# Kernel optimization log

Hardware: AMD Instinct MI355X
Metric: run time of the kernel (lower is better)

Reference implementation:

```python
import jax, jax.numpy as jnp
import numpy as np

N_NODES, N_EDGES, NUM_GRAPHS = 50000, 800000, 64
F_DIM, H_DIM, N_LAYERS, N_CLASSES = 64, 64, 3, 16
EPS = 1e-5  # StdAggregation epsilon (PyG)


def setup_inputs() -> dict:
    key = jax.random.key(0)
    ks = jax.random.split(key, 12)
    s = 0.05
    x = jax.random.normal(ks[0], (N_NODES, F_DIM), jnp.float32)
    edge_index = jax.random.randint(ks[1], (2, N_EDGES), 0, N_NODES, dtype=jnp.int32)
    batch = jnp.sort(jax.random.randint(ks[2], (N_NODES,), 0, NUM_GRAPHS, dtype=jnp.int32))
    # per-layer PNAConv params (towers=1): pre Linear(2F->F), post Linear(13F->H), lin Linear(H->H)
    pre_w = jax.random.normal(ks[3], (N_LAYERS, F_DIM, 2 * F_DIM), jnp.float32) * s
    pre_b = jnp.zeros((N_LAYERS, F_DIM), jnp.float32)
    post_w = jax.random.normal(ks[4], (N_LAYERS, H_DIM, 13 * F_DIM), jnp.float32) * s
    post_b = jnp.zeros((N_LAYERS, H_DIM), jnp.float32)
    lin_w = jax.random.normal(ks[5], (N_LAYERS, H_DIM, H_DIM), jnp.float32) * s
    lin_b = jnp.zeros((N_LAYERS, H_DIM), jnp.float32)
    mlp_w1 = jax.random.normal(ks[6], (H_DIM, H_DIM), jnp.float32) * s
    mlp_b1 = jnp.zeros((H_DIM,), jnp.float32)
    mlp_w2 = jax.random.normal(ks[7], (N_CLASSES, H_DIM), jnp.float32) * s
    mlp_b2 = jnp.zeros((N_CLASSES,), jnp.float32)
    return dict(x=x, edge_index=edge_index, batch=batch,
                pre_w=pre_w, pre_b=pre_b, post_w=post_w, post_b=post_b,
                lin_w=lin_w, lin_b=lin_b, mlp_w1=mlp_w1, mlp_b1=mlp_b1,
                mlp_w2=mlp_w2, mlp_b2=mlp_b2)


def pna_forward(x, src, dst, pre_w, pre_b, post_w, post_b, lin_w, lin_b,
                mlp_w1, mlp_b1, mlp_w2, mlp_b2, batch):
    N = x.shape[0]
    deg_raw = jax.ops.segment_sum(jnp.ones_like(src, jnp.float32), dst, N)  # in-degree [N]
    deg = jnp.maximum(deg_raw, 1.0)[:, None]
    # avg log degree (PNA avg_deg['log'] from the degree histogram of this graph)
    avg_log = jnp.mean(jnp.log(deg_raw + 1.0))
    log_deg = jnp.log(deg + 1.0)
    amp = log_deg / avg_log          # amplification scaler [N,1]
    att = avg_log / log_deg          # attenuation scaler [N,1]
    has_in = (deg_raw > 0)[:, None]

    for l in range(pre_w.shape[0]):
        h = jnp.concatenate([x[dst], x[src]], axis=-1)        # [E, 2F] (x_i, x_j)
        m = h @ pre_w[l].T + pre_b[l]                          # pre_nn message [E, F]
        s1 = jax.ops.segment_sum(m, dst, N)
        s2 = jax.ops.segment_sum(m * m, dst, N)
        mean = s1 / deg
        std = jnp.sqrt(jax.nn.relu(s2 / deg - mean * mean) + EPS)
        mn = jnp.where(has_in, jax.ops.segment_min(m, dst, N), 0.0)
        mx = jnp.where(has_in, jax.ops.segment_max(m, dst, N), 0.0)
        aggr = jnp.concatenate([mean, mn, mx, std], axis=-1)   # [N, 4F]
        out = jnp.concatenate([x, aggr, aggr * amp, aggr * att], axis=-1)  # [N, 13F]
        out = out @ post_w[l].T + post_b[l]                    # post_nn [N, H]
        x = jax.nn.relu(out @ lin_w[l].T + lin_b[l])           # conv.lin + outer ReLU

    # global mean pool over graphs
    counts = jnp.maximum(
        jax.ops.segment_sum(jnp.ones((N,), x.dtype), batch, NUM_GRAPHS), 1.0)
    g = jax.ops.segment_sum(x, batch, NUM_GRAPHS) / counts[:, None]  # [G, H]
    g = jax.nn.relu(g @ mlp_w1.T + mlp_b1)
    return g @ mlp_w2.T + mlp_b2                               # [G, C]


def reference(x, edge_index, batch, pre_w, pre_b, post_w, post_b,
              lin_w, lin_b, mlp_w1, mlp_b1, mlp_w2, mlp_b2):
    src, dst = edge_index[0], edge_index[1]
    return pna_forward(x, src, dst, pre_w, pre_b, post_w, post_b,
                       lin_w, lin_b, mlp_w1, mlp_b1, mlp_w2, mlp_b2, batch)
```

## Files before the change

kernel.cpp:

```cpp
#include <hip/hip_runtime.h>
#include <math.h>

#define N_NODES   50000
#define N_EDGES   800000
#define NUM_GRAPHS 64
#define FDIM      64
#define HDIM      64
#define NLAYERS   3
#define NCLASSES  16
#define EPS       1e-5f

#define SCAN_CHUNK 1024
#define NCHUNKS ((N_NODES + SCAN_CHUNK - 1) / SCAN_CHUNK)

typedef unsigned short u16;
typedef unsigned int   u32;
typedef __attribute__((ext_vector_type(8))) short short8;
typedef __attribute__((ext_vector_type(4))) float floatx4;

#define WKS_LAYER 159744
#define PRES_LAYER 24576

__device__ inline void split1(float f, u16& h, u16& m, u16& l) {
    u32 b  = __float_as_uint(f);
    u32 hb = b & 0xFFFF0000u;
    float r = f - __uint_as_float(hb);
    u32 mb = __float_as_uint(r) & 0xFFFF0000u;
    float r2 = r - __uint_as_float(mb);
    u32 lb = __float_as_uint(r2) & 0xFFFF0000u;
    h = (u16)(hb >> 16); m = (u16)(mb >> 16); l = (u16)(lb >> 16);
}

__device__ inline void gl_lds16(const void* g, void* l) {
    __builtin_amdgcn_global_load_lds(
        (const __attribute__((address_space(1))) u32*)g,
        (__attribute__((address_space(3))) u32*)l, 16, 0, 0);
}

__global__ __launch_bounds__(256) void k_comb(const float* __restrict__ post_w,
                                              const float* __restrict__ lin_w,
                                              const float* __restrict__ pre_w,
                                              const float* __restrict__ post_b,
                                              const float* __restrict__ lin_b,
                                              u16* __restrict__ WkS,
                                              u16* __restrict__ PreS,
                                              float* __restrict__ bcv,
                                              int* __restrict__ cnt,
                                              float* __restrict__ logsum) {
    int b = blockIdx.x, t = threadIdx.x;
    int zi = b * 256 + t;
    if (zi < N_NODES) cnt[zi] = 0;
    if (zi == 0) *logsum = 0.f;

    if (b < 624) {
        int c  = t & 63;
        int kl = t >> 6;
        int l  = b / 208;
        int o  = (b % 208) * 4 + kl;
        const float* lw = lin_w + (size_t)l * 4096 + c * 64;
        const float* pw = post_w + (size_t)l * 53248 + o;
        float acc = 0.f;
        #pragma unroll 8
        for (int j = 0; j < 64; ++j)
            acc += lw[j] * pw[(size_t)j * 832];
        u16 h, m, lo;
        split1(acc, h, m, lo);

        int kn;
        if (o < 64) kn = o;
        else {
            int s  = (o - 64) >> 8;
            int mm = (o - 64) & 255;
            int j  = mm >> 5, r = mm & 31;
            kn = 64 + j * 96 + s * 32 + r;
        }
        int ch  = kn >> 5;
        int kin = kn & 31;
        int n16 = c & 15, nt = c >> 4;
        int swk = (((kin >> 3) + (n16 >> 1)) & 3) * 8 + (kin & 7);
        size_t base = (size_t)l * WKS_LAYER + (size_t)ch * 6144
                    + nt * 512 + n16 * 32 + swk;
        WkS[base]        = h;
        WkS[base + 2048] = m;
        WkS[base + 4096] = lo;
    } else if (b == 624) {
        if (t < 192) {
            int l = t >> 6, c = t & 63;
            float acc = lin_b[l * 64 + c];
            for (int j = 0; j < 64; ++j)
                acc += lin_w[(size_t)l * 4096 + c * 64 + j] * post_b[l * 64 + j];
            bcv[l * 64 + c] = acc;
        }
    } else {
        int i = (b - 625) * 256 + t;
        int l = i >> 13;
        int rem = i & 8191;
        int c128 = rem >> 6;
        int k = rem & 63;
        float v;
        if (c128 < 64) v = pre_w[(size_t)l * 8192 + c128 * 128 + k];
        else           v = pre_w[(size_t)l * 8192 + (c128 - 64) * 128 + 64 + k];
        u16 h, m, lo;
        split1(v, h, m, lo);
        int ch = k >> 5, kin = k & 31;
        int nt = c128 >> 4, n16 = c128 & 15;
        int swk = (((kin >> 3) + (n16 >> 1)) & 3) * 8 + (kin & 7);
        size_t base = (size_t)l * PRES_LAYER + (size_t)ch * 12288
                    + nt * 512 + n16 * 32 + swk;
        PreS[base]        = h;
        PreS[base + 4096] = m;
        PreS[base + 8192] = lo;
    }
}

__global__ void k_count(const int* __restrict__ dst, int* __restrict__ cnt,
                        int* __restrict__ rank) {
    int e = blockIdx.x * 256 + threadIdx.x;
    if (e < N_EDGES) rank[e] = atomicAdd(&cnt[dst[e]], 1);
}

__global__ void k_chunk_sums(const int* __restrict__ cnt, int* __restrict__ bsum,
                             float* __restrict__ logsum) {
    __shared__ int   ired[256];
    __shared__ float lred[256];
    int b = blockIdx.x, t = threadIdx.x;
    int base = b * SCAN_CHUNK;
    int s = 0; float ls = 0.f;
    for (int i = t; i < SCAN_CHUNK; i += 256) {
        int idx = base + i;
        if (idx < N_NODES) {
            int v = cnt[idx];
            s += v;
            ls += logf((float)v + 1.0f);
        }
    }
    ired[t] = s; lred[t] = ls;
    __syncthreads();
    for (int off = 128; off > 0; off >>= 1) {
        if (t < off) { ired[t] += ired[t + off]; lred[t] += lred[t + off]; }
        __syncthreads();
    }
    if (t == 0) { bsum[b] = ired[0]; atomicAdd(logsum, lred[0]); }
}

__global__ void k_scan_top(const int* __restrict__ bsum, int* __restrict__ boff,
                           int* __restrict__ row_start) {
    if (threadIdx.x == 0) {
        int acc = 0;
        for (int i = 0; i < NCHUNKS; ++i) { boff[i] = acc; acc += bsum[i]; }
        row_start[N_NODES] = acc;
    }
}

__global__ void k_scan_chunks(const int* __restrict__ cnt, const int* __restrict__ boff,
                              int* __restrict__ row_start) {
    __shared__ int tsum[256];
    int b = blockIdx.x, t = threadIdx.x;
    int base = b * SCAN_CHUNK + t * 4;
    int v[4]; int s = 0;
    #pragma unroll
    for (int i = 0; i < 4; ++i) {
        int idx = base + i;
        v[i] = (idx < N_NODES) ? cnt[idx] : 0;
        s += v[i];
    }
    tsum[t] = s;
    __syncthreads();
    for (int off = 1; off < 256; off <<= 1) {
        int val = (t >= off) ? tsum[t - off] : 0;
        __syncthreads();
        tsum[t] += val;
        __syncthreads();
    }
    int excl = boff[b] + tsum[t] - s;
    #pragma unroll
    for (int i = 0; i < 4; ++i) {
        int idx = base + i;
        if (idx < N_NODES) row_start[idx] = excl;
        excl += v[i];
    }
}

__global__ void k_scatter(const int* __restrict__ src, const int* __restrict__ dst,
                          const int* __restrict__ rank,
                          const int* __restrict__ row_start,
                          int* __restrict__ csr_src) {
    int e = blockIdx.x * 256 + threadIdx.x;
    if (e < N_EDGES) {
        int d = dst[e];
        csr_src[row_start[d] + rank[e]] = src[e];
    }
}

__global__ void k_scal(const int* __restrict__ cnt, const float* __restrict__ logsum,
                       float* __restrict__ inv_deg, float* __restrict__ ampv,
                       float* __restrict__ attv, float* __restrict__ g_sum,
                       int* __restrict__ g_cnt) {
    int n = blockIdx.x * 256 + threadIdx.x;
    if (blockIdx.x == 0) {
        for (int i = threadIdx.x; i < 4096; i += 256) g_sum[i] = 0.f;
        if (threadIdx.x < 64) g_cnt[threadIdx.x] = 0;
    }
    if (n < N_NODES) {
        float avg = logsum[0] / (float)N_NODES;
        float degf = fmaxf((float)cnt[n], 1.0f);
        inv_deg[n] = 1.0f / degf;
        float ld = logf(degf + 1.0f);
        ampv[n] = ld / avg;
        attv[n] = avg / ld;
    }
}

__global__ __launch_bounds__(256, 4) void k_pre(const float* __restrict__ x,
                                                const u16* __restrict__ PreS,
                                                const float* __restrict__ pre_b,
                                                float* __restrict__ p,
                                                float* __restrict__ q) {
    __shared__ u16 ldsB[2 * 12288];
    int t = threadIdx.x;
    int w = t >> 6;
    int lane = t & 63;
    int m = lane & 15;
    int qh = lane >> 4;
    int rowBase = blockIdx.x * 64;

    int myrow = rowBase + 16 * w + m;
    bool vr = myrow < N_NODES;
    int crow = vr ? myrow : 0;
    const float* xrow = x + (size_t)crow * 64;

    int bo = m * 32 + ((qh + (m >> 1)) & 3) * 8;

    #pragma unroll
    for (int ch = 0; ch < 2; ++ch) {
        const char* g = (const char*)PreS + (size_t)ch * 24576 + w * 6144 + lane * 16;
        char* l = (char*)ldsB + ch * 24576 + w * 6144;
        #pragma unroll
        for (int i = 0; i < 6; ++i)
            gl_lds16(g + i * 1024, l + i * 1024);
    }
    float fa[2][8];
    #pragma unroll
    for (int ch = 0; ch < 2; ++ch) {
        const float* sp = xrow + ch * 32 + qh * 8;
        float4 u0 = *(const float4*)sp;
        float4 u1 = *(const float4*)(sp + 4);
        fa[ch][0] = vr ? u0.x : 0.f; fa[ch][1] = vr ? u0.y : 0.f;
        fa[ch][2] = vr ? u0.z : 0.f; fa[ch][3] = vr ? u0.w : 0.f;
        fa[ch][4] = vr ? u1.x : 0.f; fa[ch][5] = vr ? u1.y : 0.f;
        fa[ch][6] = vr ? u1.z : 0.f; fa[ch][7] = vr ? u1.w : 0.f;
    }
    asm volatile("s_waitcnt vmcnt(0)" ::: "memory");
    __syncthreads();

    floatx4 acc[8] = {};
    #pragma unroll
    for (int ch = 0; ch < 2; ++ch) {
        union { u32 u[4]; short8 s8; } AH, AM, AL;
        #pragma unroll
        for (int i = 0; i < 4; ++i) {
            float f0 = fa[ch][2 * i], f1 = fa[ch][2 * i + 1];
            u32 b0 = __float_as_uint(f0), b1 = __float_as_uint(f1);
            u32 h0 = b0 & 0xFFFF0000u,  h1 = b1 & 0xFFFF0000u;
            float r0 = f0 - __uint_as_float(h0);
            float r1 = f1 - __uint_as_float(h1);
            u32 m0 = __float_as_uint(r0) & 0xFFFF0000u;
            u32 m1 = __float_as_uint(r1) & 0xFFFF0000u;
            float s0 = r0 - __uint_as_float(m0);
            float s1 = r1 - __uint_as_float(m1);
            u32 l0 = __float_as_uint(s0) & 0xFFFF0000u;
            u32 l1 = __float_as_uint(s1) & 0xFFFF0000u;
            AH.u[i] = (h0 >> 16) | h1;
            AM.u[i] = (m0 >> 16) | m1;
            AL.u[i] = (l0 >> 16) | l1;
        }
        const u16* Bb = ldsB + ch * 12288;
        #pragma unroll
        for (int nt = 0; nt < 8; ++nt) {
            short8 bH = *(const short8*)(Bb + nt * 512 + bo);
            short8 bM = *(const short8*)(Bb + 4096 + nt * 512 + bo);
            short8 bL = *(const short8*)(Bb + 8192 + nt * 512 + bo);
            acc[nt] = __builtin_amdgcn_mfma_f32_16x16x32_bf16(AH.s8, bH, acc[nt], 0, 0, 0);
            acc[nt] = __builtin_amdgcn_mfma_f32_16x16x32_bf16(AH.s8, bM, acc[nt], 0, 0, 0);
            acc[nt] = __builtin_amdgcn_mfma_f32_16x16x32_bf16(AM.s8, bH, acc[nt], 0, 0, 0);
            acc[nt] = __builtin_amdgcn_mfma_f32_16x16x32_bf16(AH.s8, bL, acc[nt], 0, 0, 0);
            acc[nt] = __builtin_amdgcn_mfma_f32_16x16x32_bf16(AM.s8, bM, acc[nt], 0, 0, 0);
            acc[nt] = __builtin_amdgcn_mfma_f32_16x16x32_bf16(AL.s8, bH, acc[nt], 0, 0, 0);
        }
    }

    int col = m;
    #pragma unroll
    for (int nt = 0; nt < 8; ++nt) {
        int cbase = (nt & 3) * 16 + col;
        float bias = (nt < 4) ? pre_b[cbase] : 0.f;
        float* outp = (nt < 4) ? p : q;
        #pragma unroll
        for (int reg = 0; reg < 4; ++reg) {
            int grow = rowBase + 16 * w + qh * 4 + reg;
            if (grow < N_NODES)
                outp[(size_t)grow * 64 + cbase] = acc[nt][reg] + bias;
        }
    }
}

__global__ __launch_bounds__(256) void k_aggr(const float* __restrict__ p,
                                              const float* __restrict__ q,
                                              const int* __restrict__ row_start,
                                              const int* __restrict__ csr_src,
                                              const float* __restrict__ inv_deg,
                                              float* __restrict__ aggr) {
    int wid  = (blockIdx.x * 256 + threadIdx.x) >> 6;
    int lane = threadIdx.x & 63;
    if (wid >= N_NODES) return;
    int n = wid;
    int beg = row_start[n], end = row_start[n + 1];
    float sum = 0.f, sq = 0.f;
    float mn = INFINITY, mx = -INFINITY;
    int e = beg;
    for (; e + 7 < end; e += 8) {
        float qv[8];
        #pragma unroll
        for (int u = 0; u < 8; ++u) {
            int s = csr_src[e + u];
            qv[u] = q[(size_t)s * 64 + lane];
        }
        #pragma unroll
        for (int u = 0; u < 8; ++u) {
            float m = qv[u];
            sum += m; sq += m * m;
            mn = fminf(mn, m); mx = fmaxf(mx, m);
        }
    }
    for (; e + 3 < end; e += 4) {
        float qv[4];
        #pragma unroll
        for (int u = 0; u < 4; ++u) {
            int s = csr_src[e + u];
            qv[u] = q[(size_t)s * 64 + lane];
        }
        #pragma unroll
        for (int u = 0; u < 4; ++u) {
            float m = qv[u];
            sum += m; sq += m * m;
            mn = fminf(mn, m); mx = fmaxf(mx, m);
        }
    }
    for (; e < end; ++e) {
        int s = csr_src[e];
        float m = q[(size_t)s * 64 + lane];
        sum += m; sq += m * m;
        mn = fminf(mn, m); mx = fmaxf(mx, m);
    }
    float* a = aggr + (size_t)n * 256;
    if (end <= beg) {
        a[lane]       = 0.f;
        a[64 + lane]  = 0.f;
        a[128 + lane] = 0.f;
        a[192 + lane] = sqrtf(EPS);
    } else {
        float pv = p[n * 64 + lane];
        float id = inv_deg[n];
        float meanq = sum * id;
        float var = fmaxf(sq * id - meanq * meanq, 0.f);
        a[lane]       = pv + meanq;
        a[64 + lane]  = pv + mn;
        a[128 + lane] = pv + mx;
        a[192 + lane] = sqrtf(var + EPS);
    }
}

__global__ __launch_bounds__(256, 4) void k_post(const float* __restrict__ x,
                                                 const float* __restrict__ aggr,
                                                 const float* __restrict__ ampv,
                                                 const float* __restrict__ attv,
                                                 const u16* __restrict__ WkS,
                                                 const float* __restrict__ bc,
                                                 float* __restrict__ xout) {
    __shared__ u16 ldsB[3 * 6144];
    int t = threadIdx.x;
    int w = t >> 6;
    int lane = t & 63;
    int m = lane & 15;
    int qh = lane >> 4;
    int rowBase = blockIdx.x * 64;

    int myrow = rowBase + 16 * w + m;
    bool vr = myrow < N_NODES;
    int crow = vr ? myrow : 0;
    float ampR = vr ? ampv[crow] : 0.f;
    float attR = vr ? attv[crow] : 0.f;
    const float* xrow = x + (size_t)crow * 64;
    const float* arow = aggr + (size_t)crow * 256;

    int bo = m * 32 + ((qh + (m >> 1)) & 3) * 8;

    floatx4 acc[4] = {};
    float fc[8], fn[8];

    auto aptr = [&](int ch) -> const float* {
        if (ch <= 0) return xrow;
        if (ch == 1) return xrow + 32;
        int j = (ch - 2) / 3;
        if (j > 7) j = 7;
        return arow + j * 32;
    };
    auto loadRaw = [&](const float* sp, float* f) {
        float4 u0 = *(const float4*)(sp + qh * 8);
        float4 u1 = *(const float4*)(sp + qh * 8 + 4);
        f[0] = vr ? u0.x : 0.f; f[1] = vr ? u0.y : 0.f;
        f[2] = vr ? u0.z : 0.f; f[3] = vr ? u0.w : 0.f;
        f[4] = vr ? u1.x : 0.f; f[5] = vr ? u1.y : 0.f;
        f[6] = vr ? u1.z : 0.f; f[7] = vr ? u1.w : 0.f;
    };
    auto stageIssue = [&](int ch, int buf) {
        const char* g = (const char*)WkS + (size_t)ch * 12288 + w * 3072 + lane * 16;
        char* l = (char*)ldsB + buf * 12288 + w * 3072;
        #pragma unroll
        for (int i = 0; i < 3; ++i)
            gl_lds16(g + i * 1024, l + i * 1024);
    };

    loadRaw(aptr(0), fc);
    stageIssue(0, 0);
    stageIssue(1, 1);
    asm volatile("s_waitcnt vmcnt(3)" ::: "memory");
    asm volatile("s_barrier" ::: "memory");

    for (int ch = 0; ch < 26; ++ch) {
        loadRaw(aptr(ch + 1), fn);
        int ch2 = (ch + 2 < 26) ? ch + 2 : ch + 2 - 26;
        stageIssue(ch2, (ch + 2) % 3);

        float sc = 1.f;
        if (ch >= 2) {
            int s = (ch - 2) % 3;
            sc = (s == 0) ? 1.f : ((s == 1) ? ampR : attR);
        }

        union { u32 u[4]; short8 s8; } AH, AM, AL;
        #pragma unroll
        for (int i = 0; i < 4; ++i) {
            float f0 = fc[2 * i] * sc, f1 = fc[2 * i + 1] * sc;
            u32 b0 = __float_as_uint(f0), b1 = __float_as_uint(f1);
            u32 h0 = b0 & 0xFFFF0000u,  h1 = b1 & 0xFFFF0000u;
            float r0 = f0 - __uint_as_float(h0);
            float r1 = f1 - __uint_as_float(h1);
            u32 m0 = __float_as_uint(r0) & 0xFFFF0000u;
            u32 m1 = __float_as_uint(r1) & 0xFFFF0000u;
            float s0 = r0 - __uint_as_float(m0);
            float s1 = r1 - __uint_as_float(m1);
            u32 l0 = __float_as_uint(s0) & 0xFFFF0000u;
            u32 l1 = __float_as_uint(s1) & 0xFFFF0000u;
            AH.u[i] = (h0 >> 16) | h1;
            AM.u[i] = (m0 >> 16) | m1;
            AL.u[i] = (l0 >> 16) | l1;
        }

        const u16* Bb = ldsB + (ch % 3) * 6144;
        #pragma unroll
        for (int nt = 0; nt < 4; ++nt) {
            short8 bH = *(const short8*)(Bb + nt * 512 + bo);
            short8 bM = *(const short8*)(Bb + 2048 + nt * 512 + bo);
            short8 bL = *(const short8*)(Bb + 4096 + nt * 512 + bo);
            acc[nt] = __builtin_amdgcn_mfma_f32_16x16x32_bf16(AH.s8, bH, acc[nt], 0, 0, 0);
            acc[nt] = __builtin_amdgcn_mfma_f32_16x16x32_bf16(AH.s8, bM, acc[nt], 0, 0, 0);
            acc[nt] = __builtin_amdgcn_mfma_f32_16x16x32_bf16(AM.s8, bH, acc[nt], 0, 0, 0);
            acc[nt] = __builtin_amdgcn_mfma_f32_16x16x32_bf16(AH.s8, bL, acc[nt], 0, 0, 0);
            acc[nt] = __builtin_amdgcn_mfma_f32_16x16x32_bf16(AM.s8, bM, acc[nt], 0, 0, 0);
            acc[nt] = __builtin_amdgcn_mfma_f32_16x16x32_bf16(AL.s8, bH, acc[nt], 0, 0, 0);
        }

        asm volatile("s_waitcnt vmcnt(5)" ::: "memory");
        asm volatile("s_barrier" ::: "memory");

        #pragma unroll
        for (int i = 0; i < 8; ++i) fc[i] = fn[i];
    }

    int col = lane & 15;
    #pragma unroll
    for (int nt = 0; nt < 4; ++nt) {
        float bias = bc[nt * 16 + col];
        #pragma unroll
        for (int reg = 0; reg < 4; ++reg) {
            int grow = rowBase + 16 * w + qh * 4 + reg;
            if (grow < N_NODES) {
                xout[(size_t)grow * 64 + nt * 16 + col] =
                    fmaxf(acc[nt][reg] + bias, 0.f);
            }
        }
    }
}

__global__ __launch_bounds__(256) void k_pool(const float* __restrict__ x,
                                              const int* __restrict__ batch,
                                              float* __restrict__ g_sum,
                                              int* __restrict__ g_cnt) {
    int lane = threadIdx.x & 63;
    int wave = blockIdx.x * 4 + (threadIdx.x >> 6);
    const int NPW = 16;
    int beg = wave * NPW;
    if (beg >= N_NODES) return;
    int end = min(beg + NPW, N_NODES);
    float acc = 0.f;
    int cur = batch[beg];
    int c = 0;
    for (int n = beg; n < end; ++n) {
        int b = batch[n];
        if (b != cur) {
            atomicAdd(&g_sum[cur * 64 + lane], acc);
            if (lane == 0) atomicAdd(&g_cnt[cur], c);
            acc = 0.f; c = 0; cur = b;
        }
        acc += x[n * 64 + lane];
        ++c;
    }
    atomicAdd(&g_sum[cur * 64 + lane], acc);
    if (lane == 0) atomicAdd(&g_cnt[cur], c);
}

__global__ __launch_bounds__(256) void k_mlp(const float* __restrict__ g_sum,
                                             const int* __restrict__ g_cnt,
                                             const float* __restrict__ w1,
                                             const float* __restrict__ b1,
                                             const float* __restrict__ w2,
                                             const float* __restrict__ b2,
                                             float* __restrict__ out) {
    __shared__ float g[64][64];
    __shared__ float h[64][64];
    __shared__ float wT[64][65];
    int t = threadIdx.x;
    for (int idx = t; idx < 4096; idx += 256) {
        int gi = idx >> 6, c = idx & 63;
        float cntf = fmaxf((float)g_cnt[gi], 1.f);
        g[gi][c] = g_sum[idx] / cntf;
    }
    for (int idx = t; idx < 4096; idx += 256) {
        int c = idx >> 6, k = idx & 63;
        wT[k][c] = w1[c * 64 + k];
    }
    __syncthreads();
    for (int idx = t; idx < 4096; idx += 256) {
        int gi = idx >> 6, c = idx & 63;
        float acc = b1[c];
        for (int k = 0; k < 64; ++k) acc += g[gi][k] * wT[k][c];
        h[gi][c] = fmaxf(acc, 0.f);
    }
    __syncthreads();
    for (int idx = t; idx < 64 * NCLASSES; idx += 256) {
        int gi = idx >> 4, c = idx & 15;
        float acc = b2[c];
        for (int k = 0; k < 64; ++k) acc += h[gi][k] * w2[c * 64 + k];
        out[gi * NCLASSES + c] = acc;
    }
}

extern "C" void kernel_launch(void* const* d_in, const int* in_sizes, int n_in,
                              void* d_out, int out_size, void* d_ws, size_t ws_size,
                              hipStream_t stream) {
    const float* x      = (const float*)d_in[0];
    const int*   ei     = (const int*)d_in[1];
    const int*   batch  = (const int*)d_in[2];
    const float* pre_w  = (const float*)d_in[3];
    const float* pre_b  = (const float*)d_in[4];
    const float* post_w = (const float*)d_in[5];
    const float* post_b = (const float*)d_in[6];
    const float* lin_w  = (const float*)d_in[7];
    const float* lin_b  = (const float*)d_in[8];
    const float* mlp_w1 = (const float*)d_in[9];
    const float* mlp_b1 = (const float*)d_in[10];
    const float* mlp_w2 = (const float*)d_in[11];
    const float* mlp_b2 = (const float*)d_in[12];

    const int* src = ei;
    const int* dst = ei + N_EDGES;

    char* base = (char*)d_ws;
    size_t off = 0;
    auto alloc = [&](size_t bytes) -> void* {
        void* ptr = base + off;
        off += (bytes + 255) & ~(size_t)255;
        return ptr;
    };
    int*   cnt       = (int*)alloc(N_NODES * 4);
    int*   row_start = (int*)alloc((N_NODES + 1) * 4);
    int*   rank      = (int*)alloc(N_EDGES * 4);
    int*   csr_src   = (int*)alloc(N_EDGES * 4);
    int*   bsum      = (int*)alloc(64 * 4);
    int*   boff      = (int*)alloc(64 * 4);
    float* logsum    = (float*)alloc(16);
    float* inv_deg   = (float*)alloc(N_NODES * 4);
    float* ampv      = (float*)alloc(N_NODES * 4);
    float* attv      = (float*)alloc(N_NODES * 4);
    float* p         = (float*)alloc((size_t)N_NODES * 64 * 4);
    float* q         = (float*)alloc((size_t)N_NODES * 64 * 4);
    float* aggr      = (float*)alloc((size_t)N_NODES * 256 * 4);
    float* xb0       = (float*)alloc((size_t)N_NODES * 64 * 4);
    float* xb1       = (float*)alloc((size_t)N_NODES * 64 * 4);
    float* g_sum     = (float*)alloc(64 * 64 * 4);
    int*   g_cnt     = (int*)alloc(64 * 4);
    u16*   WkS       = (u16*)alloc((size_t)3 * WKS_LAYER * 2);
    u16*   PreS      = (u16*)alloc((size_t)3 * PRES_LAYER * 2);
    float* bcv       = (float*)alloc(3 * 64 * 4);

    k_comb<<<721, 256, 0, stream>>>(post_w, lin_w, pre_w, post_b, lin_b,
                                    WkS, PreS, bcv, cnt, logsum);

    k_count<<<(N_EDGES + 255) / 256, 256, 0, stream>>>(dst, cnt, rank);
    k_chunk_sums<<<NCHUNKS, 256, 0, stream>>>(cnt, bsum, logsum);
    k_scan_top<<<1, 64, 0, stream>>>(bsum, boff, row_start);
    k_scan_chunks<<<NCHUNKS, 256, 0, stream>>>(cnt, boff, row_start);
    k_scatter<<<(N_EDGES + 255) / 256, 256, 0, stream>>>(src, dst, rank,
                                                         row_start, csr_src);
    k_scal<<<(N_NODES + 255) / 256, 256, 0, stream>>>(cnt, logsum, inv_deg,
                                                      ampv, attv, g_sum, g_cnt);

    const int GEMM_BLOCKS = (N_NODES + 63) / 64;
    const float* xin = x;
    float* bufs[3] = {xb0, xb1, xb0};
    for (int l = 0; l < NLAYERS; ++l) {
        k_pre<<<GEMM_BLOCKS, 256, 0, stream>>>(xin, PreS + (size_t)l * PRES_LAYER,
                                               pre_b + l * 64, p, q);
        k_aggr<<<(N_NODES + 3) / 4, 256, 0, stream>>>(p, q, row_start, csr_src,
                                                      inv_deg, aggr);
        float* xo = bufs[l];
        k_post<<<GEMM_BLOCKS, 256, 0, stream>>>(xin, aggr, ampv, attv,
                                                WkS + (size_t)l * WKS_LAYER,
                                                bcv + l * 64, xo);
        xin = xo;
    }

    int pool_waves = (N_NODES + 15) / 16;
    k_pool<<<(pool_waves + 3) / 4, 256, 0, stream>>>(xin, batch, g_sum, g_cnt);
    k_mlp<<<1, 256, 0, stream>>>(g_sum, g_cnt, mlp_w1, mlp_b1, mlp_w2, mlp_b2,
                                 (float*)d_out);
}
```

Before: 477.8 us.

## Process two row fragments per wave in post GEMM and defer scaler multiply

The post-aggregation GEMM kernel now handles 128 rows per block, two 16-row fragments per wave, so each staged weight tile in LDS is reused for twice as many rows. The amp/att scaling is no longer applied to the A operand before the bf16 split. Instead three separate accumulators (plain, amp, att) are kept and combined with the per-row scalers in the epilogue, so each aggregate chunk is loaded and split once rather than three times. This raises register pressure (six accumulator arrays), so launch bounds drop to 2 blocks per CU, which may reduce occupancy and latency hiding.

New measurement: 482.3 us. No clear change (+0.9%).

```diff
diff --git a/kernel.cpp b/kernel.cpp
--- a/kernel.cpp
+++ b/kernel.cpp
@@ -370,7 +370,29 @@
     }
 }
 
-__global__ __launch_bounds__(256, 4) void k_post(const float* __restrict__ x,
+#define DOMFMA(ACC0, ACC1)                                                     \
+    {                                                                          \
+        _Pragma("unroll")                                                      \
+        for (int nt = 0; nt < 4; ++nt) {                                       \
+            short8 bH = *(const short8*)(Bb + nt * 512 + bo);                  \
+            short8 bM = *(const short8*)(Bb + 2048 + nt * 512 + bo);           \
+            short8 bL = *(const short8*)(Bb + 4096 + nt * 512 + bo);           \
+            ACC0[nt] = __builtin_amdgcn_mfma_f32_16x16x32_bf16(AH0.s8, bH, ACC0[nt], 0, 0, 0); \
+            ACC0[nt] = __builtin_amdgcn_mfma_f32_16x16x32_bf16(AH0.s8, bM, ACC0[nt], 0, 0, 0); \
+            ACC0[nt] = __builtin_amdgcn_mfma_f32_16x16x32_bf16(AM0.s8, bH, ACC0[nt], 0, 0, 0); \
+            ACC0[nt] = __builtin_amdgcn_mfma_f32_16x16x32_bf16(AH0.s8, bL, ACC0[nt], 0, 0, 0); \
+            ACC0[nt] = __builtin_amdgcn_mfma_f32_16x16x32_bf16(AM0.s8, bM, ACC0[nt], 0, 0, 0); \
+            ACC0[nt] = __builtin_amdgcn_mfma_f32_16x16x32_bf16(AL0.s8, bH, ACC0[nt], 0, 0, 0); \
+            ACC1[nt] = __builtin_amdgcn_mfma_f32_16x16x32_bf16(AH1.s8, bH, ACC1[nt], 0, 0, 0); \
+            ACC1[nt] = __builtin_amdgcn_mfma_f32_16x16x32_bf16(AH1.s8, bM, ACC1[nt], 0, 0, 0); \
+            ACC1[nt] = __builtin_amdgcn_mfma_f32_16x16x32_bf16(AM1.s8, bH, ACC1[nt], 0, 0, 0); \
+            ACC1[nt] = __builtin_amdgcn_mfma_f32_16x16x32_bf16(AH1.s8, bL, ACC1[nt], 0, 0, 0); \
+            ACC1[nt] = __builtin_amdgcn_mfma_f32_16x16x32_bf16(AM1.s8, bM, ACC1[nt], 0, 0, 0); \
+            ACC1[nt] = __builtin_amdgcn_mfma_f32_16x16x32_bf16(AL1.s8, bH, ACC1[nt], 0, 0, 0); \
+        }                                                                      \
+    }
+
+__global__ __launch_bounds__(256, 2) void k_post(const float* __restrict__ x,
                                                  const float* __restrict__ aggr,
                                                  const float* __restrict__ ampv,
                                                  const float* __restrict__ attv,
@@ -383,35 +405,34 @@
     int lane = t & 63;
     int m = lane & 15;
     int qh = lane >> 4;
-    int rowBase = blockIdx.x * 64;
-
-    int myrow = rowBase + 16 * w + m;
-    bool vr = myrow < N_NODES;
-    int crow = vr ? myrow : 0;
-    float ampR = vr ? ampv[crow] : 0.f;
-    float attR = vr ? attv[crow] : 0.f;
-    const float* xrow = x + (size_t)crow * 64;
-    const float* arow = aggr + (size_t)crow * 256;
+    int rowBase = blockIdx.x * 128;
+
+    int row0 = rowBase + 32 * w + m;
+    int row1 = row0 + 16;
+    int cr0 = (row0 < N_NODES) ? row0 : 0;
+    int cr1 = (row1 < N_NODES) ? row1 : 0;
+    const float* xr0 = x + (size_t)cr0 * 64;
+    const float* xr1 = x + (size_t)cr1 * 64;
+    const float* ar0 = aggr + (size_t)cr0 * 256;
+    const float* ar1 = aggr + (size_t)cr1 * 256;
 
     int bo = m * 32 + ((qh + (m >> 1)) & 3) * 8;
 
-    floatx4 acc[4] = {};
-    float fc[8], fn[8];
-
-    auto aptr = [&](int ch) -> const float* {
-        if (ch <= 0) return xrow;
-        if (ch == 1) return xrow + 32;
-        int j = (ch - 2) / 3;
-        if (j > 7) j = 7;
-        return arow + j * 32;
+    floatx4 accP0[4] = {}, accA0[4] = {}, accT0[4] = {};
+    floatx4 accP1[4] = {}, accA1[4] = {}, accT1[4] = {};
+
+    float f0[8], f1[8];
+    union U8 { u32 u[4]; short8 s8; };
+    U8 AH0, AM0, AL0, AH1, AM1, AL1;
+
+    auto gptr = [&](int g, const float* xr, const float* ar) -> const float* {
+        return (g < 2) ? (xr + 32 * g) : (ar + (g - 2) * 32);
     };
     auto loadRaw = [&](const float* sp, float* f) {
         float4 u0 = *(const float4*)(sp + qh * 8);
         float4 u1 = *(const float4*)(sp + qh * 8 + 4);
-        f[0] = vr ? u0.x : 0.f; f[1] = vr ? u0.y : 0.f;
-        f[2] = vr ? u0.z : 0.f; f[3] = vr ? u0.w : 0.f;
-        f[4] = vr ? u1.x : 0.f; f[5] = vr ? u1.y : 0.f;
-        f[6] = vr ? u1.z : 0.f; f[7] = vr ? u1.w : 0.f;
+        f[0] = u0.x; f[1] = u0.y; f[2] = u0.z; f[3] = u0.w;
+        f[4] = u1.x; f[5] = u1.y; f[6] = u1.z; f[7] = u1.w;
     };
     auto stageIssue = [&](int ch, int buf) {
         const char* g = (const char*)WkS + (size_t)ch * 12288 + w * 3072 + lane * 16;
@@ -420,78 +441,79 @@
         for (int i = 0; i < 3; ++i)
             gl_lds16(g + i * 1024, l + i * 1024);
     };
-
-    loadRaw(aptr(0), fc);
-    stageIssue(0, 0);
-    stageIssue(1, 1);
-    asm volatile("s_waitcnt vmcnt(3)" ::: "memory");
-    asm volatile("s_barrier" ::: "memory");
-
-    for (int ch = 0; ch < 26; ++ch) {
-        loadRaw(aptr(ch + 1), fn);
-        int ch2 = (ch + 2 < 26) ? ch + 2 : ch + 2 - 26;
-        stageIssue(ch2, (ch + 2) % 3);
-
-        float sc = 1.f;
-        if (ch >= 2) {
-            int s = (ch - 2) % 3;
-            sc = (s == 0) ? 1.f : ((s == 1) ? ampR : attR);
-        }
-
-        union { u32 u[4]; short8 s8; } AH, AM, AL;
+    auto split2 = [&](const float* f, U8& H, U8& M8, U8& L) {
         #pragma unroll
         for (int i = 0; i < 4; ++i) {
-            float f0 = fc[2 * i] * sc, f1 = fc[2 * i + 1] * sc;
-            u32 b0 = __float_as_uint(f0), b1 = __float_as_uint(f1);
+            float v0 = f[2 * i], v1 = f[2 * i + 1];
+            u32 b0 = __float_as_uint(v0), b1 = __float_as_uint(v1);
             u32 h0 = b0 & 0xFFFF0000u,  h1 = b1 & 0xFFFF0000u;
-            float r0 = f0 - __uint_as_float(h0);
-            float r1 = f1 - __uint_as_float(h1);
+            float r0 = v0 - __uint_as_float(h0);
+            float r1 = v1 - __uint_as_float(h1);
             u32 m0 = __float_as_uint(r0) & 0xFFFF0000u;
             u32 m1 = __float_as_uint(r1) & 0xFFFF0000u;
             float s0 = r0 - __uint_as_float(m0);
             float s1 = r1 - __uint_as_float(m1);
             u32 l0 = __float_as_uint(s0) & 0xFFFF0000u;
             u32 l1 = __float_as_uint(s1) & 0xFFFF0000u;
-            AH.u[i] = (h0 >> 16) | h1;
-            AM.u[i] = (m0 >> 16) | m1;
-            AL.u[i] = (l0 >> 16) | l1;
-        }
+            H.u[i]  = (h0 >> 16) | h1;
+            M8.u[i] = (m0 >> 16) | m1;
+            L.u[i]  = (l0 >> 16) | l1;
+        }
+    };
+
+    loadRaw(gptr(0, xr0, ar0), f0);
+    loadRaw(gptr(0, xr1, ar1), f1);
+    stageIssue(0, 0);
+    stageIssue(1, 1);
+    asm volatile("s_waitcnt vmcnt(3)" ::: "memory");
+    asm volatile("s_barrier" ::: "memory");
+
+    for (int ch = 0; ch < 26; ++ch) {
+        int s = (ch < 2) ? 0 : (ch - 2) % 3;
+        if (s == 0) {
+            split2(f0, AH0, AM0, AL0);
+            split2(f1, AH1, AM1, AL1);
+        }
+        bool pf = (ch + 1 < 26) && ((ch + 1 < 2) || ((ch + 1 - 2) % 3 == 0));
+        if (pf) {
+            int gn = (ch + 1 < 2) ? (ch + 1) : (2 + (ch + 1 - 2) / 3);
+            loadRaw(gptr(gn, xr0, ar0), f0);
+            loadRaw(gptr(gn, xr1, ar1), f1);
+        }
+        int ch2 = (ch + 2 < 26) ? ch + 2 : ch + 2 - 26;
+        stageIssue(ch2, (ch + 2) % 3);
 
         const u16* Bb = ldsB + (ch % 3) * 6144;
-        #pragma unroll
-        for (int nt = 0; nt < 4; ++nt) {
-            short8 bH = *(const short8*)(Bb + nt * 512 + bo);
-            short8 bM = *(const short8*)(Bb + 2048 + nt * 512 + bo);
-            short8 bL = *(const short8*)(Bb + 4096 + nt * 512 + bo);
-            acc[nt] = __builtin_amdgcn_mfma_f32_16x16x32_bf16(AH.s8, bH, acc[nt], 0, 0, 0);
-            acc[nt] = __builtin_amdgcn_mfma_f32_16x16x32_bf16(AH.s8, bM, acc[nt], 0, 0, 0);
-            acc[nt] = __builtin_amdgcn_mfma_f32_16x16x32_bf16(AM.s8, bH, acc[nt], 0, 0, 0);
-            acc[nt] = __builtin_amdgcn_mfma_f32_16x16x32_bf16(AH.s8, bL, acc[nt], 0, 0, 0);
-            acc[nt] = __builtin_amdgcn_mfma_f32_16x16x32_bf16(AM.s8, bM, acc[nt], 0, 0, 0);
-            acc[nt] = __builtin_amdgcn_mfma_f32_16x16x32_bf16(AL.s8, bH, acc[nt], 0, 0, 0);
-        }
-
-        asm volatile("s_waitcnt vmcnt(5)" ::: "memory");
+        if (s == 0)      { DOMFMA(accP0, accP1); }
+        else if (s == 1) { DOMFMA(accA0, accA1); }
+        else             { DOMFMA(accT0, accT1); }
+
+        if (pf) asm volatile("s_waitcnt vmcnt(7)" ::: "memory");
+        else    asm volatile("s_waitcnt vmcnt(3)" ::: "memory");
         asm volatile("s_barrier" ::: "memory");
-
-        #pragma unroll
-        for (int i = 0; i < 8; ++i) fc[i] = fn[i];
-    }
-
-    int col = lane & 15;
+    }
+
+    int col = m;
     #pragma unroll
-    for (int nt = 0; nt < 4; ++nt) {
-        float bias = bc[nt * 16 + col];
+    for (int frag = 0; frag < 2; ++frag) {
         #pragma unroll
         for (int reg = 0; reg < 4; ++reg) {
-            int grow = rowBase + 16 * w + qh * 4 + reg;
+            int grow = rowBase + 32 * w + 16 * frag + qh * 4 + reg;
             if (grow < N_NODES) {
-                xout[(size_t)grow * 64 + nt * 16 + col] =
-                    fmaxf(acc[nt][reg] + bias, 0.f);
+                float av = ampv[grow], tv = attv[grow];
+                #pragma unroll
+                for (int nt = 0; nt < 4; ++nt) {
+                    float pv = frag ? accP1[nt][reg] : accP0[nt][reg];
+                    float av2 = frag ? accA1[nt][reg] : accA0[nt][reg];
+                    float tv2 = frag ? accT1[nt][reg] : accT0[nt][reg];
+                    float v = pv + av * av2 + tv * tv2 + bc[nt * 16 + col];
+                    xout[(size_t)grow * 64 + nt * 16 + col] = fmaxf(v, 0.f);
+                }
             }
         }
     }
 }
+#undef DOMFMA
 
 __global__ __launch_bounds__(256) void k_pool(const float* __restrict__ x,
                                               const int* __restrict__ batch,
@@ -616,16 +638,17 @@
     k_scal<<<(N_NODES + 255) / 256, 256, 0, stream>>>(cnt, logsum, inv_deg,
                                                       ampv, attv, g_sum, g_cnt);
 
-    const int GEMM_BLOCKS = (N_NODES + 63) / 64;
+    const int PRE_BLOCKS  = (N_NODES + 63) / 64;
+    const int POST_BLOCKS = (N_NODES + 127) / 128;
     const float* xin = x;
     float* bufs[3] = {xb0, xb1, xb0};
     for (int l = 0; l < NLAYERS; ++l) {
-        k_pre<<<GEMM_BLOCKS, 256, 0, stream>>>(xin, PreS + (size_t)l * PRES_LAYER,
-                                               pre_b + l * 64, p, q);
+        k_pre<<<PRE_BLOCKS, 256, 0, stream>>>(xin, PreS + (size_t)l * PRES_LAYER,
+                                              pre_b + l * 64, p, q);
         k_aggr<<<(N_NODES + 3) / 4, 256, 0, stream>>>(p, q, row_start, csr_src,
                                                       inv_deg, aggr);
         float* xo = bufs[l];
-        k_post<<<GEMM_BLOCKS, 256, 0, stream>>>(xin, aggr, ampv, attv,
+        k_post<<<POST_BLOCKS, 256, 0, stream>>>(xin, aggr, ampv, attv,
                                                 WkS + (size_t)l * WKS_LAYER,
                                                 bcv + l * 64, xo);
         xin = xo;
```
